# Kernel tuning notes

Measured on AMD Instinct MI355X. Metric: run time of the kernel, lower is better.

The kernel has to match this reference:

```python
import jax, jax.numpy as jnp
import numpy as np

EPS = 1e-7
ALPHA = 16.0
RANK = 64
CURV = 1.0


def lorentz_expmap0(x, c):
    # x: [N, d] tangent at origin (spatial part). Returns [N, d+1] point on hyperboloid.
    sc = jnp.sqrt(c)
    vn = jnp.maximum(jnp.linalg.norm(x, axis=-1, keepdims=True), EPS)  # [N,1]
    t = jnp.cosh(sc * vn) / sc                                        # [N,1] time coord
    sp = (jnp.sinh(sc * vn) / (sc * vn)) * x                          # [N,d] spatial
    return jnp.concatenate([t, sp], axis=-1)


def lorentz_recompute_time(s, c):
    # s: [N, d] spatial part. time = sqrt(1/c + ||s||^2) so <p,p>_L = -1/c.
    sq = jnp.sum(s * s, axis=-1, keepdims=True)
    t = jnp.sqrt(1.0 / c + sq)
    return jnp.concatenate([t, s], axis=-1)


def lorentz_logmap0(p, c):
    # p: [N, d+1] on hyperboloid. Returns [N, d] tangent (spatial) at origin.
    sc = jnp.sqrt(c)
    t = p[:, :1]
    y = p[:, 1:]
    yn = jnp.maximum(jnp.linalg.norm(y, axis=-1, keepdims=True), EPS)
    arg = jnp.maximum(sc * t, 1.0 + EPS)  # arccosh domain clamp
    d = jnp.arccosh(arg) / sc             # geodesic distance from origin
    return (d / yn) * y


def setup_inputs() -> dict:
    key = jax.random.key(0)
    k1, k2, k3 = jax.random.split(key, 3)
    N, D_IN, D_OUT, R = 16384, 4096, 4096, RANK
    x = jax.random.normal(k1, (N, D_IN), dtype=jnp.float32) * 0.02
    # torch Linear weight layout: A_w [r, in], B_w [out, r]
    A_w = jax.random.normal(k2, (R, D_IN), dtype=jnp.float32) * (1.0 / np.sqrt(D_IN))
    B_w = jax.random.normal(k3, (D_OUT, R), dtype=jnp.float32) * (1.0 / np.sqrt(R))
    return {"x": x, "A_w": A_w, "B_w": B_w}


def reference(x, A_w, B_w):
    c = CURV
    p0 = lorentz_expmap0(x, c)                    # [N, D_IN+1]
    s1 = p0[:, 1:] @ A_w.T                        # [N, R]
    p1 = lorentz_recompute_time(s1, c)            # [N, R+1]
    s2 = p1[:, 1:] @ B_w.T                        # [N, D_OUT]
    p2 = lorentz_recompute_time(s2, c)            # [N, D_OUT+1]
    v = lorentz_logmap0(p2, c)                    # [N, D_OUT]
    return (ALPHA / RANK) * v
```

## Files before the change

### kernel.cpp

```cpp
#include <hip/hip_runtime.h>
#include <hip/hip_bf16.h>

#define NROWS 16384
#define DIN   4096
#define DOUT  4096
#define RNK   64
#define EPSF  1e-7f

typedef float  f32x4  __attribute__((ext_vector_type(4)));
typedef __bf16 bf16x4 __attribute__((ext_vector_type(4)));
typedef __bf16 bf16x8 __attribute__((ext_vector_type(8)));

__device__ __forceinline__ bf16x8 cvt8(f32x4 a, f32x4 b) {
    bf16x8 r;
    r[0]=(__bf16)a.x; r[1]=(__bf16)a.y; r[2]=(__bf16)a.z; r[3]=(__bf16)a.w;
    r[4]=(__bf16)b.x; r[5]=(__bf16)b.y; r[6]=(__bf16)b.z; r[7]=(__bf16)b.w;
    return r;
}
__device__ __forceinline__ bf16x4 cvt4(f32x4 v) {
    bf16x4 r;
    r[0]=(__bf16)v.x; r[1]=(__bf16)v.y; r[2]=(__bf16)v.z; r[3]=(__bf16)v.w;
    return r;
}

__global__ __launch_bounds__(512, 2)
void ka_apf(const float* __restrict__ Aw, __bf16* __restrict__ Apf) {
    const int kt = blockIdx.x;
    const int t = threadIdx.x;
    const int ng = t >> 7, le = (t >> 1) & 63, h = t & 1;
    f32x4 v = *(const f32x4*)&Aw[(size_t)(ng*16 + (le&15)) * DIN + kt*32 + (le>>4)*8 + h*4];
    *(bf16x4*)&Apf[((size_t)(kt*4 + ng))*512 + le*8 + h*4] = cvt4(v);
}

__global__ __launch_bounds__(512, 4)
void kb_gram(const float* __restrict__ Bw, __bf16* __restrict__ Bpf,
             float* __restrict__ Gpart) {
    __shared__ __bf16 bs[256][72];
    const int t = threadIdx.x;
    const int jb = blockIdx.x * 256;

    {
        const int j0 = t >> 1, c0 = (t & 1) * 32;
        #pragma unroll
        for (int u = 0; u < 4; ++u) {
            f32x4 v0 = *(const f32x4*)&Bw[(size_t)(jb + j0) * RNK + c0 + 8*u];
            f32x4 v1 = *(const f32x4*)&Bw[(size_t)(jb + j0) * RNK + c0 + 8*u + 4];
            *(bf16x8*)&bs[j0][c0 + 8*u] = cvt8(v0, v1);
        }
    }
    __syncthreads();

    #pragma unroll
    for (int u = 0; u < 4; ++u) {
        const int lc = t + 512 * u;
        const int ll = lc & 63;
        const int ks = (lc >> 6) & 1;
        const int jl = lc >> 7;
        bf16x8 v = *(const bf16x8*)&bs[jl * 16 + (ll & 15)][ks * 32 + (ll >> 4) * 8];
        const size_t C = ((size_t)((jb >> 4) + jl) * 2 + ks) * 64 + ll;
        *(bf16x8*)&Bpf[C * 8] = v;
    }

    const int r = t & 63, rp = (t >> 6) * 8;
    float acc[8] = {0,0,0,0,0,0,0,0};
    for (int j = 0; j < 256; ++j) {
        float s = (float)bs[j][r];
        bf16x8 v = *(const bf16x8*)&bs[j][rp];
        #pragma unroll
        for (int u = 0; u < 8; ++u) acc[u] += s * (float)v[u];
    }
    #pragma unroll
    for (int u = 0; u < 8; ++u)
        Gpart[(size_t)blockIdx.x * 4096 + r * 64 + rp + u] = acc[u];
}

__global__ void kc0_sum(const float* __restrict__ Gpart, float* __restrict__ G) {
    const int t = threadIdx.x;
    #pragma unroll
    for (int v = 0; v < 4; ++v) {
        f32x4 a = {0.f, 0.f, 0.f, 0.f};
        for (int b = 0; b < 16; ++b)
            a += *(const f32x4*)&Gpart[(size_t)b * 4096 + t * 16 + v * 4];
        *(f32x4*)&G[t * 16 + v * 4] = a;
    }
}

__global__ __launch_bounds__(256, 4)
void k1(const float* __restrict__ x, const __bf16* __restrict__ Apf,
        const float* __restrict__ G, __bf16* __restrict__ s1pf) {
    __shared__ float part[4][16][68];
    __shared__ float Gs[64][64];
    __shared__ float s1s[16][68];
    __shared__ float ssqs[4][16];
    __shared__ float gsl[16];

    const int t = threadIdx.x, l = t & 63, w = t >> 6;
    const int brow = blockIdx.x * 16;
    const int rl = l & 15, ko = l >> 4;

    const size_t xoff = (size_t)(brow + rl) * DIN + (size_t)w * 1024 + ko * 8;
    const size_t aoff = (size_t)(w * 32) * 2048 + (size_t)l * 8;

    f32x4 acc0 = {0,0,0,0}, acc1 = {0,0,0,0}, acc2 = {0,0,0,0}, acc3 = {0,0,0,0};
    float ssq = 0.f;

    f32x4 xc0 = *(const f32x4*)&x[xoff];
    f32x4 xc1 = *(const f32x4*)&x[xoff + 4];
    bf16x8 a0 = *(const bf16x8*)&Apf[aoff];
    bf16x8 a1 = *(const bf16x8*)&Apf[aoff + 512];
    bf16x8 a2 = *(const bf16x8*)&Apf[aoff + 1024];
    bf16x8 a3 = *(const bf16x8*)&Apf[aoff + 1536];

    #pragma unroll
    for (int i = 0; i < 32; ++i) {
        f32x4 xn0 = xc0, xn1 = xc1;
        bf16x8 b0 = a0, b1 = a1, b2 = a2, b3 = a3;
        if (i < 31) {
            xn0 = *(const f32x4*)&x[xoff + (i+1)*32];
            xn1 = *(const f32x4*)&x[xoff + (i+1)*32 + 4];
            const size_t ao = aoff + (size_t)(i+1)*2048;
            b0 = *(const bf16x8*)&Apf[ao];
            b1 = *(const bf16x8*)&Apf[ao + 512];
            b2 = *(const bf16x8*)&Apf[ao + 1024];
            b3 = *(const bf16x8*)&Apf[ao + 1536];
        }
        ssq += xc0.x*xc0.x + xc0.y*xc0.y + xc0.z*xc0.z + xc0.w*xc0.w;
        ssq += xc1.x*xc1.x + xc1.y*xc1.y + xc1.z*xc1.z + xc1.w*xc1.w;
        bf16x8 xf = cvt8(xc0, xc1);
        acc0 = __builtin_amdgcn_mfma_f32_16x16x32_bf16(a0, xf, acc0, 0, 0, 0);
        acc1 = __builtin_amdgcn_mfma_f32_16x16x32_bf16(a1, xf, acc1, 0, 0, 0);
        acc2 = __builtin_amdgcn_mfma_f32_16x16x32_bf16(a2, xf, acc2, 0, 0, 0);
        acc3 = __builtin_amdgcn_mfma_f32_16x16x32_bf16(a3, xf, acc3, 0, 0, 0);
        xc0 = xn0; xc1 = xn1; a0 = b0; a1 = b1; a2 = b2; a3 = b3;
    }

    *(f32x4*)&part[w][rl][ 0 + ko*4] = acc0;
    *(f32x4*)&part[w][rl][16 + ko*4] = acc1;
    *(f32x4*)&part[w][rl][32 + ko*4] = acc2;
    *(f32x4*)&part[w][rl][48 + ko*4] = acc3;
    ssq += __shfl_xor(ssq, 16);
    ssq += __shfl_xor(ssq, 32);
    if (l < 16) ssqs[w][l] = ssq;
    {
        float* gf = &Gs[0][0];
        const float* gp = &G[t * 16];
        *(f32x4*)&gf[t*16 + 0]  = *(const f32x4*)&gp[0];
        *(f32x4*)&gf[t*16 + 4]  = *(const f32x4*)&gp[4];
        *(f32x4*)&gf[t*16 + 8]  = *(const f32x4*)&gp[8];
        *(f32x4*)&gf[t*16 + 12] = *(const f32x4*)&gp[12];
    }
    __syncthreads();

    const int row = t >> 4, c4 = (t & 15) * 4;
    f32x4 s = *(const f32x4*)&part[0][row][c4];
    s += *(const f32x4*)&part[1][row][c4];
    s += *(const f32x4*)&part[2][row][c4];
    s += *(const f32x4*)&part[3][row][c4];
    const float ssqt = ssqs[0][row] + ssqs[1][row] + ssqs[2][row] + ssqs[3][row];
    const float vn = fmaxf(sqrtf(ssqt), EPSF);
    const float sc = sinhf(vn) / vn;
    s *= sc;
    *(f32x4*)&s1s[row][c4] = s;
    __syncthreads();

    f32x4 yacc = {0,0,0,0};
    for (int j = 0; j < 64; ++j) {
        const float sj = s1s[row][j];
        yacc += *(const f32x4*)&Gs[j][c4] * sj;
    }
    float r2p = s.x*yacc.x + s.y*yacc.y + s.z*yacc.z + s.w*yacc.w;
    r2p += __shfl_xor(r2p, 1);
    r2p += __shfl_xor(r2p, 2);
    r2p += __shfl_xor(r2p, 4);
    r2p += __shfl_xor(r2p, 8);
    if ((t & 15) == 0) {
        const float r2 = r2p;
        const float rn = sqrtf(r2);
        gsl[row] = 0.25f * acoshf(fmaxf(sqrtf(1.f + r2), 1.f + EPSF))
                         / fmaxf(rn, EPSF);
    }
    __syncthreads();

    if (t < 128) {
        const int le = t & 63, ks = t >> 6;
        const int er = le & 15, ec = ks * 32 + (le >> 4) * 8;
        const float g = gsl[er];
        bf16x8 p;
        #pragma unroll
        for (int u = 0; u < 8; ++u) p[u] = (__bf16)(g * s1s[er][ec + u]);
        *(bf16x8*)&s1pf[((size_t)(blockIdx.x * 2 + ks) * 64 + le) * 8] = p;
    }
}

__global__ __launch_bounds__(256, 4)
void k2(const __bf16* __restrict__ s1pf, const __bf16* __restrict__ Bpf,
        float* __restrict__ out) {
    const int t = threadIdx.x, l = t & 63, w = t >> 6;
    const int rt = blockIdx.x >> 6;
    const int ct = blockIdx.x & 63;
    const int g16 = rt * 4 + w;

    const bf16x8 sf0 = *(const bf16x8*)&s1pf[((size_t)(g16*2 + 0) * 64 + l) * 8];
    const bf16x8 sf1 = *(const bf16x8*)&s1pf[((size_t)(g16*2 + 1) * 64 + l) * 8];

    f32x4 acc[4];
    #pragma unroll
    for (int ng = 0; ng < 4; ++ng) {
        const size_t base = ((size_t)((ct*4 + ng)*2) * 64 + l) * 8;
        bf16x8 b0 = *(const bf16x8*)&Bpf[base];
        bf16x8 b1 = *(const bf16x8*)&Bpf[base + 512];
        f32x4 a = {0.f, 0.f, 0.f, 0.f};
        a = __builtin_amdgcn_mfma_f32_16x16x32_bf16(b0, sf0, a, 0, 0, 0);
        a = __builtin_amdgcn_mfma_f32_16x16x32_bf16(b1, sf1, a, 0, 0, 0);
        acc[ng] = a;
    }

    const int orow = rt * 64 + w * 16 + (l & 15);
    const size_t ob = (size_t)orow * DOUT + ct * 64 + (l >> 4) * 4;
    #pragma unroll
    for (int ng = 0; ng < 4; ++ng)
        *(f32x4*)&out[ob + ng * 16] = acc[ng];
}

extern "C" void kernel_launch(void* const* d_in, const int* in_sizes, int n_in,
                              void* d_out, int out_size, void* d_ws, size_t ws_size,
                              hipStream_t stream) {
    const float* x  = (const float*)d_in[0];
    const float* Aw = (const float*)d_in[1];
    const float* Bw = (const float*)d_in[2];
    float* out = (float*)d_out;

    char* ws = (char*)d_ws;
    __bf16* Apf   = (__bf16*)(ws);
    __bf16* Bpf   = (__bf16*)(ws + 0x080000);
    float*  Gpart = (float*)(ws + 0x100000);
    float*  G     = (float*)(ws + 0x140000);
    __bf16* s1pf  = (__bf16*)(ws + 0x150000);

    ka_apf<<<128, 512, 0, stream>>>(Aw, Apf);
    kb_gram<<<16, 512, 0, stream>>>(Bw, Bpf, Gpart);
    kc0_sum<<<1, 256, 0, stream>>>(Gpart, G);
    k1<<<NROWS / 16, 256, 0, stream>>>(x, Apf, G, s1pf);
    k2<<<16384, 256, 0, stream>>>(s1pf, Bpf, out);
}
```

Before: 178.6 us.

## Fuse rank-projection and output GEMM kernels, keeping s1 in shared memory

Merges k1 and k2 into one kernel. Each 16-row block now writes its scaled bf16 s1 fragments into shared memory, which aliases the now-free partial-sum buffer, and then loops over all 256 output column tiles, split across its four waves, to compute and store the output. This removes the global round-trip of s1 and one kernel launch. In exchange the output-writing phase runs with only 1024 blocks instead of 16384 and stores a 16x16 tile per iteration, so store parallelism and latency hiding may suffer. Bpf is re-read by every block, but it is small and should stay in cache.

```diff
diff --git a/kernel.cpp b/kernel.cpp
--- a/kernel.cpp
+++ b/kernel.cpp
@@ -86,13 +86,16 @@
 }
 
 __global__ __launch_bounds__(256, 4)
-void k1(const float* __restrict__ x, const __bf16* __restrict__ Apf,
-        const float* __restrict__ G, __bf16* __restrict__ s1pf) {
-    __shared__ float part[4][16][68];
-    __shared__ float Gs[64][64];
-    __shared__ float s1s[16][68];
-    __shared__ float ssqs[4][16];
-    __shared__ float gsl[16];
+void kfused(const float* __restrict__ x, const __bf16* __restrict__ Apf,
+            const float* __restrict__ G, const __bf16* __restrict__ Bpf,
+            float* __restrict__ out) {
+    __shared__ __align__(16) char smem[38464];
+    float (*part)[16][68] = (float (*)[16][68])(smem);
+    float (*Gs)[64]       = (float (*)[64])(smem + 17408);
+    float (*s1s)[68]      = (float (*)[68])(smem + 33792);
+    float (*ssqs)[16]     = (float (*)[16])(smem + 38144);
+    float *gsl            = (float*)(smem + 38400);
+    __bf16 (*s1pf)[64][8] = (__bf16 (*)[64][8])(smem);
 
     const int t = threadIdx.x, l = t & 63, w = t >> 6;
     const int brow = blockIdx.x * 16;
@@ -188,38 +191,26 @@
         bf16x8 p;
         #pragma unroll
         for (int u = 0; u < 8; ++u) p[u] = (__bf16)(g * s1s[er][ec + u]);
-        *(bf16x8*)&s1pf[((size_t)(blockIdx.x * 2 + ks) * 64 + le) * 8] = p;
-    }
-}
-
-__global__ __launch_bounds__(256, 4)
-void k2(const __bf16* __restrict__ s1pf, const __bf16* __restrict__ Bpf,
-        float* __restrict__ out) {
-    const int t = threadIdx.x, l = t & 63, w = t >> 6;
-    const int rt = blockIdx.x >> 6;
-    const int ct = blockIdx.x & 63;
-    const int g16 = rt * 4 + w;
-
-    const bf16x8 sf0 = *(const bf16x8*)&s1pf[((size_t)(g16*2 + 0) * 64 + l) * 8];
-    const bf16x8 sf1 = *(const bf16x8*)&s1pf[((size_t)(g16*2 + 1) * 64 + l) * 8];
-
-    f32x4 acc[4];
-    #pragma unroll
-    for (int ng = 0; ng < 4; ++ng) {
-        const size_t base = ((size_t)((ct*4 + ng)*2) * 64 + l) * 8;
-        bf16x8 b0 = *(const bf16x8*)&Bpf[base];
-        bf16x8 b1 = *(const bf16x8*)&Bpf[base + 512];
-        f32x4 a = {0.f, 0.f, 0.f, 0.f};
-        a = __builtin_amdgcn_mfma_f32_16x16x32_bf16(b0, sf0, a, 0, 0, 0);
-        a = __builtin_amdgcn_mfma_f32_16x16x32_bf16(b1, sf1, a, 0, 0, 0);
-        acc[ng] = a;
-    }
-
-    const int orow = rt * 64 + w * 16 + (l & 15);
-    const size_t ob = (size_t)orow * DOUT + ct * 64 + (l >> 4) * 4;
-    #pragma unroll
-    for (int ng = 0; ng < 4; ++ng)
-        *(f32x4*)&out[ob + ng * 16] = acc[ng];
+        *(bf16x8*)&s1pf[ks][le][0] = p;
+    }
+    __syncthreads();
+
+    {
+        const bf16x8 sf0 = *(const bf16x8*)&s1pf[0][l][0];
+        const bf16x8 sf1 = *(const bf16x8*)&s1pf[1][l][0];
+        const size_t orow = (size_t)(brow + rl) * DOUT + ko * 4;
+        #pragma unroll 4
+        for (int jj = 0; jj < 64; ++jj) {
+            const int j = w * 64 + jj;
+            const size_t base = (size_t)j * 1024 + l * 8;
+            bf16x8 b0 = *(const bf16x8*)&Bpf[base];
+            bf16x8 b1 = *(const bf16x8*)&Bpf[base + 512];
+            f32x4 a = {0.f, 0.f, 0.f, 0.f};
+            a = __builtin_amdgcn_mfma_f32_16x16x32_bf16(b0, sf0, a, 0, 0, 0);
+            a = __builtin_amdgcn_mfma_f32_16x16x32_bf16(b1, sf1, a, 0, 0, 0);
+            *(f32x4*)&out[orow + (size_t)j * 16] = a;
+        }
+    }
 }
 
 extern "C" void kernel_launch(void* const* d_in, const int* in_sizes, int n_in,
@@ -235,11 +226,9 @@
     __bf16* Bpf   = (__bf16*)(ws + 0x080000);
     float*  Gpart = (float*)(ws + 0x100000);
     float*  G     = (float*)(ws + 0x140000);
-    __bf16* s1pf  = (__bf16*)(ws + 0x150000);
 
     ka_apf<<<128, 512, 0, stream>>>(Aw, Apf);
     kb_gram<<<16, 512, 0, stream>>>(Bw, Bpf, Gpart);
     kc0_sum<<<1, 256, 0, stream>>>(Gpart, G);
-    k1<<<NROWS / 16, 256, 0, stream>>>(x, Apf, G, s1pf);
-    k2<<<16384, 256, 0, stream>>>(s1pf, Bpf, out);
-}
+    kfused<<<NROWS / 16, 256, 0, stream>>>(x, Apf, G, Bpf, out);
+}
```

Result: slower. 208.9 us (+17.0%).
